# Optimization experiments

Hardware: AMD Instinct MI355X
Metric: run time of the kernel (lower is better)

The kernel has to match this reference:

```python
import jax, jax.numpy as jnp
import numpy as np

N_INST = 524288   # total instances across all bags
NF = 256          # feature dim
L = 128           # gated-attention hidden dim
C = 1             # num_classes
B = 4096          # num bags


def setup_inputs() -> dict:
    key = jax.random.key(0)
    k = jax.random.split(key, 6)
    # ragged bag sizes averaging ~128, deterministically summing to N_INST
    rng = np.random.RandomState(0)
    raw = rng.randint(64, 193, size=B).astype(np.int64)
    sizes = (raw * N_INST // raw.sum()).astype(np.int64)
    sizes[: int(N_INST - sizes.sum())] += 1  # distribute remainder (< B)
    assert sizes.sum() == N_INST
    s = 1.0 / np.sqrt(NF)
    return {
        "feats": jax.random.normal(k[0], (N_INST, NF), jnp.float32),
        "split_sizes": jnp.asarray(sizes, jnp.int64),
        "W_ins": jax.random.normal(k[1], (NF, C), jnp.float32) * s,
        "b_ins": jnp.zeros((C,), jnp.float32),
        "W_V": jax.random.normal(k[2], (NF, L), jnp.float32) * s,
        "b_V": jnp.zeros((L,), jnp.float32),
        "W_U": jax.random.normal(k[3], (NF, L), jnp.float32) * s,
        "b_U": jnp.zeros((L,), jnp.float32),
        "w_att": jax.random.normal(k[4], (L, 1), jnp.float32) * (1.0 / np.sqrt(L)),
        "b_att": jnp.zeros((1,), jnp.float32),
    }


def reference(feats, split_sizes, W_ins, b_ins, W_V, b_V, W_U, b_U, w_att, b_att):
    n = feats.shape[0]
    num_bags = split_sizes.shape[0]
    # segment id per instance (fused replacement of torch.split + Python loop)
    seg = jnp.repeat(jnp.arange(num_bags), split_sizes, total_repeat_length=n)

    # instance classifier (applied once to the whole ragged batch)
    inst_pred = feats @ W_ins + b_ins                      # [N, C]

    # gated attention scores
    gate = jnp.tanh(feats @ W_V + b_V) * jax.nn.sigmoid(feats @ W_U + b_U)
    scores = (gate @ w_att + b_att)[:, 0]                  # [N]

    # segmented softmax over each bag
    m = jax.ops.segment_max(scores, seg, num_segments=num_bags)  # [B]
    e = jnp.exp(scores - m[seg])
    denom = jax.ops.segment_sum(e, seg, num_segments=num_bags)   # [B]
    attn = e / denom[seg]                                        # [N]

    # bag prediction = attention-weighted sum of instance predictions
    bag_pred = jax.ops.segment_sum(attn[:, None] * inst_pred, seg,
                                   num_segments=num_bags)        # [B, C]
    return bag_pred, inst_pred
```

## Files before the change

### kernel.cpp

```cpp
#include <hip/hip_runtime.h>
#include <hip/hip_bf16.h>

#define N_INST 524288
#define NF     256
#define LDIM   128
#define NBAGS  4096
#define BM     128

typedef __attribute__((ext_vector_type(8)))  short          short8;
typedef __attribute__((ext_vector_type(16))) float          f32x16;
typedef __attribute__((ext_vector_type(4)))  unsigned short ushort4v;
typedef __attribute__((ext_vector_type(4)))  int            int4v;

__device__ __forceinline__ unsigned short f2bf(float f) {
    unsigned u = __float_as_uint(f);
    unsigned r = u + 0x7FFFu + ((u >> 16) & 1u);
    return (unsigned short)(r >> 16);
}

__global__ __launch_bounds__(256) void k_build(const float* __restrict__ W_V,
                                               const float* __restrict__ W_U,
                                               unsigned short* __restrict__ Bws) {
    int idx  = blockIdx.x * 256 + threadIdx.x;
    int j    = idx & 7;
    int lane = (idx >> 3) & 63;
    int ct   = (idx >> 9) & 7;
    int ks   = idx >> 12;
    int k    = ks * 16 + ((lane >> 5) << 3) + j;
    int n    = ((ct >> 1) << 5) + (lane & 31);
    const float* src = (ct & 1) ? W_U : W_V;
    Bws[idx] = f2bf(src[k * LDIM + n]);
}

__global__ __launch_bounds__(256) void k_scan(const int* __restrict__ sraw,
                                              int* __restrict__ offs) {
    __shared__ int csum[256];
    __shared__ int cpref[256];
    const int t = threadIdx.x;
    const bool is64 = (sraw[1] == 0);
    int local[16];
    int ssum = 0;
    for (int j = 0; j < 16; ++j) {
        int i = t * 16 + j;
        int v = is64 ? sraw[2 * i] : sraw[i];
        local[j] = v;
        ssum += v;
    }
    csum[t] = ssum;
    __syncthreads();
    if (t == 0) {
        int run = 0;
        for (int i = 0; i < 256; ++i) { cpref[i] = run; run += csum[i]; }
    }
    __syncthreads();
    int run = cpref[t];
    for (int j = 0; j < 16; ++j) { offs[t * 16 + j] = run; run += local[j]; }
    if (t == 255) offs[NBAGS] = run;
}

__global__ __launch_bounds__(256, 2) void k_gemm(
    const float* __restrict__ feats, const unsigned short* __restrict__ Bws,
    const float* __restrict__ W_ins, const float* __restrict__ b_ins,
    const float* __restrict__ b_V,   const float* __restrict__ b_U,
    const float* __restrict__ w_att, const float* __restrict__ b_att,
    float* __restrict__ scores, float* __restrict__ inst_out) {

    __shared__ unsigned short Al[2][2048];
    __shared__ unsigned short Bl[2][4096];
    __shared__ float winsl[NF];
    __shared__ float bVl[LDIM], bUl[LDIM], wal[LDIM];
    __shared__ float Sp[BM][4];

    const int t    = threadIdx.x;
    const int lane = t & 63;
    const int cg   = t >> 6;
    const long r0  = (long)blockIdx.x * BM;

    const int row0 = t >> 2;
    const int q    = t & 3;
    const int row1 = row0 + 64;

    winsl[t] = W_ins[t];
    if (t < LDIM) { bVl[t] = b_V[t]; bUl[t] = b_U[t]; wal[t] = w_att[t]; }

    const float* arow0 = feats + (r0 + row0) * NF + q * 4;
    const float* arow1 = feats + (r0 + row1) * NF + q * 4;
    const int4v* bsrc  = (const int4v*)Bws;

    const int aoff0 = ((row0 >> 5) * 64 + (q >> 1) * 32 + (row0 & 31)) * 8 + (q & 1) * 4;
    const int aoff1 = ((row1 >> 5) * 64 + (q >> 1) * 32 + (row1 & 31)) * 8 + (q & 1) * 4;

    float4 pa0_0 = *(const float4*)(arow0);
    float4 pa1_0 = *(const float4*)(arow1);
    int4v  pb0_0 = bsrc[t];
    int4v  pb1_0 = bsrc[t + 256];
    float4 pa0_1 = *(const float4*)(arow0 + 16);
    float4 pa1_1 = *(const float4*)(arow1 + 16);
    int4v  pb0_1 = bsrc[512 + t];
    int4v  pb1_1 = bsrc[512 + t + 256];

    f32x16 accV0 = {}, accV1 = {}, accV2 = {}, accV3 = {};
    f32x16 accU0 = {}, accU1 = {}, accU2 = {}, accU3 = {};
    float pacc0 = 0.f, pacc1 = 0.f;

    __syncthreads();

    #pragma unroll
    for (int ks = 0; ks < 16; ++ks) {
        float4 av0 = (ks & 1) ? pa0_1 : pa0_0;
        float4 av1 = (ks & 1) ? pa1_1 : pa1_0;
        int4v  bv0 = (ks & 1) ? pb0_1 : pb0_0;
        int4v  bv1 = (ks & 1) ? pb1_1 : pb1_0;
        const int X = ks & 1;

        float4 wv = *(const float4*)&winsl[ks * 16 + q * 4];
        pacc0 += av0.x * wv.x + av0.y * wv.y + av0.z * wv.z + av0.w * wv.w;
        pacc1 += av1.x * wv.x + av1.y * wv.y + av1.z * wv.z + av1.w * wv.w;

        ushort4v c0, c1;
        c0.x = f2bf(av0.x); c0.y = f2bf(av0.y); c0.z = f2bf(av0.z); c0.w = f2bf(av0.w);
        c1.x = f2bf(av1.x); c1.y = f2bf(av1.y); c1.z = f2bf(av1.z); c1.w = f2bf(av1.w);
        *(ushort4v*)&Al[X][aoff0] = c0;
        *(ushort4v*)&Al[X][aoff1] = c1;
        ((int4v*)Bl[X])[t]       = bv0;
        ((int4v*)Bl[X])[t + 256] = bv1;

        if (ks < 14) {
            if (X == 0) {
                pa0_0 = *(const float4*)(arow0 + (ks + 2) * 16);
                pa1_0 = *(const float4*)(arow1 + (ks + 2) * 16);
                pb0_0 = bsrc[(ks + 2) * 512 + t];
                pb1_0 = bsrc[(ks + 2) * 512 + t + 256];
            } else {
                pa0_1 = *(const float4*)(arow0 + (ks + 2) * 16);
                pa1_1 = *(const float4*)(arow1 + (ks + 2) * 16);
                pb0_1 = bsrc[(ks + 2) * 512 + t];
                pb1_1 = bsrc[(ks + 2) * 512 + t + 256];
            }
        }

        __syncthreads();

        short8 fa0 = *(const short8*)&Al[X][(0 * 64 + lane) * 8];
        short8 fa1 = *(const short8*)&Al[X][(1 * 64 + lane) * 8];
        short8 fa2 = *(const short8*)&Al[X][(2 * 64 + lane) * 8];
        short8 fa3 = *(const short8*)&Al[X][(3 * 64 + lane) * 8];
        short8 fbv = *(const short8*)&Bl[X][((cg * 2 + 0) * 64 + lane) * 8];
        short8 fbu = *(const short8*)&Bl[X][((cg * 2 + 1) * 64 + lane) * 8];
        accV0 = __builtin_amdgcn_mfma_f32_32x32x16_bf16(fa0, fbv, accV0, 0, 0, 0);
        accU0 = __builtin_amdgcn_mfma_f32_32x32x16_bf16(fa0, fbu, accU0, 0, 0, 0);
        accV1 = __builtin_amdgcn_mfma_f32_32x32x16_bf16(fa1, fbv, accV1, 0, 0, 0);
        accU1 = __builtin_amdgcn_mfma_f32_32x32x16_bf16(fa1, fbu, accU1, 0, 0, 0);
        accV2 = __builtin_amdgcn_mfma_f32_32x32x16_bf16(fa2, fbv, accV2, 0, 0, 0);
        accU2 = __builtin_amdgcn_mfma_f32_32x32x16_bf16(fa2, fbu, accU2, 0, 0, 0);
        accV3 = __builtin_amdgcn_mfma_f32_32x32x16_bf16(fa3, fbv, accV3, 0, 0, 0);
        accU3 = __builtin_amdgcn_mfma_f32_32x32x16_bf16(fa3, fbu, accU3, 0, 0, 0);
    }

    const int   c32 = lane & 31;
    const int   nn  = cg * 32 + c32;
    const float bv0s = bVl[nn], bu0s = bUl[nn], wn = wal[nn];
    const int   rh  = lane >> 5;

#define EPILOG(RT, AV, AU)                                                    \
    {                                                                         \
        _Pragma("unroll")                                                     \
        for (int r = 0; r < 16; ++r) {                                        \
            float v  = AV[r] + bv0s;                                          \
            float u  = AU[r] + bu0s;                                          \
            float ev = __expf(2.f * v);                                       \
            float th = 1.f - 2.f * __builtin_amdgcn_rcpf(ev + 1.f);           \
            float sg = __builtin_amdgcn_rcpf(1.f + __expf(-u));               \
            float x  = th * sg * wn;                                          \
            x += __shfl_xor(x, 1);                                            \
            x += __shfl_xor(x, 2);                                            \
            x += __shfl_xor(x, 4);                                            \
            x += __shfl_xor(x, 8);                                            \
            x += __shfl_xor(x, 16);                                           \
            if (c32 == 0)                                                     \
                Sp[RT * 32 + (r & 3) + 8 * (r >> 2) + 4 * rh][cg] = x;        \
        }                                                                     \
    }
    EPILOG(0, accV0, accU0)
    EPILOG(1, accV1, accU1)
    EPILOG(2, accV2, accU2)
    EPILOG(3, accV3, accU3)
#undef EPILOG

    float pt0 = pacc0;
    pt0 += __shfl_xor(pt0, 1);
    pt0 += __shfl_xor(pt0, 2);
    float pt1 = pacc1;
    pt1 += __shfl_xor(pt1, 1);
    pt1 += __shfl_xor(pt1, 2);
    if (q == 0) {
        float bi = b_ins[0];
        inst_out[r0 + row0] = pt0 + bi;
        inst_out[r0 + row1] = pt1 + bi;
    }

    __syncthreads();
    if (t < BM)
        scores[r0 + t] = Sp[t][0] + Sp[t][1] + Sp[t][2] + Sp[t][3] + b_att[0];
}

__global__ __launch_bounds__(64) void k_bags(const int* __restrict__ offs,
                                             const float* __restrict__ scores,
                                             const float* __restrict__ inst,
                                             float* __restrict__ bag_out) {
    const int b    = blockIdx.x;
    const int lane = threadIdx.x;
    const int s0 = offs[b], s1 = offs[b + 1];
    float m = -1e30f;
    for (int i = s0 + lane; i < s1; i += 64) m = fmaxf(m, scores[i]);
    #pragma unroll
    for (int d = 32; d; d >>= 1) m = fmaxf(m, __shfl_xor(m, d));
    float se = 0.f, sp = 0.f;
    for (int i = s0 + lane; i < s1; i += 64) {
        float e = __expf(scores[i] - m);
        se += e;
        sp += e * inst[i];
    }
    #pragma unroll
    for (int d = 32; d; d >>= 1) { se += __shfl_xor(se, d); sp += __shfl_xor(sp, d); }
    if (lane == 0) bag_out[b] = sp / se;
}

extern "C" void kernel_launch(void* const* d_in, const int* in_sizes, int n_in,
                              void* d_out, int out_size, void* d_ws, size_t ws_size,
                              hipStream_t stream) {
    const float* feats  = (const float*)d_in[0];
    const int*   sizesr = (const int*)d_in[1];
    const float* W_ins  = (const float*)d_in[2];
    const float* b_ins  = (const float*)d_in[3];
    const float* W_V    = (const float*)d_in[4];
    const float* b_V    = (const float*)d_in[5];
    const float* W_U    = (const float*)d_in[6];
    const float* b_U    = (const float*)d_in[7];
    const float* w_att  = (const float*)d_in[8];
    const float* b_att  = (const float*)d_in[9];

    unsigned short* Bws    = (unsigned short*)d_ws;
    int*            offs   = (int*)((char*)d_ws + (128 << 10));
    float*          scores = (float*)((char*)d_ws + (160 << 10));

    float* bag_out  = (float*)d_out;
    float* inst_out = (float*)d_out + NBAGS;

    hipLaunchKernelGGL(k_build, dim3(256), dim3(256), 0, stream, W_V, W_U, Bws);
    hipLaunchKernelGGL(k_scan,  dim3(1),   dim3(256), 0, stream, sizesr, offs);
    hipLaunchKernelGGL(k_gemm,  dim3(N_INST / BM), dim3(256), 0, stream,
                       feats, Bws, W_ins, b_ins, b_V, b_U, w_att, b_att,
                       scores, inst_out);
    hipLaunchKernelGGL(k_bags,  dim3(NBAGS), dim3(64), 0, stream,
                       offs, scores, inst_out, bag_out);
}
```

Before: 886.1 us.

## Halve GEMM row tile and load B fragments directly from global into registers

The row tile of the fused gated-attention GEMM drops from 128 to 64 instances per block. Each wave now loads its bf16 weight fragments straight from global memory into registers, with no shared-memory B staging, and occupancy is raised to 3 blocks per SIMD. This removes the LDS traffic and stores for B, lowers accumulator register pressure, and doubles the grid to improve latency hiding. In exchange, weight reuse per block is halved, so more global/L2 reads of B are needed per instance.

```diff
diff --git a/kernel.cpp b/kernel.cpp
--- a/kernel.cpp
+++ b/kernel.cpp
@@ -5,7 +5,7 @@
 #define NF     256
 #define LDIM   128
 #define NBAGS  4096
-#define BM     128
+#define BM     64
 
 typedef __attribute__((ext_vector_type(8)))  short          short8;
 typedef __attribute__((ext_vector_type(16))) float          f32x16;
@@ -58,15 +58,14 @@
     if (t == 255) offs[NBAGS] = run;
 }
 
-__global__ __launch_bounds__(256, 2) void k_gemm(
+__global__ __launch_bounds__(256, 3) void k_gemm(
     const float* __restrict__ feats, const unsigned short* __restrict__ Bws,
     const float* __restrict__ W_ins, const float* __restrict__ b_ins,
     const float* __restrict__ b_V,   const float* __restrict__ b_U,
     const float* __restrict__ w_att, const float* __restrict__ b_att,
     float* __restrict__ scores, float* __restrict__ inst_out) {
 
-    __shared__ unsigned short Al[2][2048];
-    __shared__ unsigned short Bl[2][4096];
+    __shared__ unsigned short Al[2][1024];
     __shared__ float winsl[NF];
     __shared__ float bVl[LDIM], bUl[LDIM], wal[LDIM];
     __shared__ float Sp[BM][4];
@@ -76,66 +75,55 @@
     const int cg   = t >> 6;
     const long r0  = (long)blockIdx.x * BM;
 
-    const int row0 = t >> 2;
-    const int q    = t & 3;
-    const int row1 = row0 + 64;
+    const int row = t >> 2;
+    const int q   = t & 3;
 
     winsl[t] = W_ins[t];
     if (t < LDIM) { bVl[t] = b_V[t]; bUl[t] = b_U[t]; wal[t] = w_att[t]; }
 
-    const float* arow0 = feats + (r0 + row0) * NF + q * 4;
-    const float* arow1 = feats + (r0 + row1) * NF + q * 4;
-    const int4v* bsrc  = (const int4v*)Bws;
-
-    const int aoff0 = ((row0 >> 5) * 64 + (q >> 1) * 32 + (row0 & 31)) * 8 + (q & 1) * 4;
-    const int aoff1 = ((row1 >> 5) * 64 + (q >> 1) * 32 + (row1 & 31)) * 8 + (q & 1) * 4;
-
-    float4 pa0_0 = *(const float4*)(arow0);
-    float4 pa1_0 = *(const float4*)(arow1);
-    int4v  pb0_0 = bsrc[t];
-    int4v  pb1_0 = bsrc[t + 256];
-    float4 pa0_1 = *(const float4*)(arow0 + 16);
-    float4 pa1_1 = *(const float4*)(arow1 + 16);
-    int4v  pb0_1 = bsrc[512 + t];
-    int4v  pb1_1 = bsrc[512 + t + 256];
-
-    f32x16 accV0 = {}, accV1 = {}, accV2 = {}, accV3 = {};
-    f32x16 accU0 = {}, accU1 = {}, accU2 = {}, accU3 = {};
-    float pacc0 = 0.f, pacc1 = 0.f;
+    const float*  arow = feats + (r0 + row) * NF + q * 4;
+    const short8* bw   = (const short8*)Bws;
+
+    const int aoff = ((row >> 5) * 64 + (q >> 1) * 32 + (row & 31)) * 8 + (q & 1) * 4;
+    const int ctv  = cg * 2;
+    const int ctu  = ctv + 1;
+
+    float4 pa_0  = *(const float4*)(arow);
+    short8 fbv_0 = bw[(0 * 8 + ctv) * 64 + lane];
+    short8 fbu_0 = bw[(0 * 8 + ctu) * 64 + lane];
+    float4 pa_1  = *(const float4*)(arow + 16);
+    short8 fbv_1 = bw[(1 * 8 + ctv) * 64 + lane];
+    short8 fbu_1 = bw[(1 * 8 + ctu) * 64 + lane];
+
+    f32x16 accV0 = {}, accV1 = {};
+    f32x16 accU0 = {}, accU1 = {};
+    float pacc = 0.f;
 
     __syncthreads();
 
     #pragma unroll
     for (int ks = 0; ks < 16; ++ks) {
-        float4 av0 = (ks & 1) ? pa0_1 : pa0_0;
-        float4 av1 = (ks & 1) ? pa1_1 : pa1_0;
-        int4v  bv0 = (ks & 1) ? pb0_1 : pb0_0;
-        int4v  bv1 = (ks & 1) ? pb1_1 : pb1_0;
         const int X = ks & 1;
+        float4 av  = X ? pa_1  : pa_0;
+        short8 fbv = X ? fbv_1 : fbv_0;
+        short8 fbu = X ? fbu_1 : fbu_0;
 
         float4 wv = *(const float4*)&winsl[ks * 16 + q * 4];
-        pacc0 += av0.x * wv.x + av0.y * wv.y + av0.z * wv.z + av0.w * wv.w;
-        pacc1 += av1.x * wv.x + av1.y * wv.y + av1.z * wv.z + av1.w * wv.w;
-
-        ushort4v c0, c1;
-        c0.x = f2bf(av0.x); c0.y = f2bf(av0.y); c0.z = f2bf(av0.z); c0.w = f2bf(av0.w);
-        c1.x = f2bf(av1.x); c1.y = f2bf(av1.y); c1.z = f2bf(av1.z); c1.w = f2bf(av1.w);
-        *(ushort4v*)&Al[X][aoff0] = c0;
-        *(ushort4v*)&Al[X][aoff1] = c1;
-        ((int4v*)Bl[X])[t]       = bv0;
-        ((int4v*)Bl[X])[t + 256] = bv1;
+        pacc += av.x * wv.x + av.y * wv.y + av.z * wv.z + av.w * wv.w;
+
+        ushort4v c;
+        c.x = f2bf(av.x); c.y = f2bf(av.y); c.z = f2bf(av.z); c.w = f2bf(av.w);
+        *(ushort4v*)&Al[X][aoff] = c;
 
         if (ks < 14) {
             if (X == 0) {
-                pa0_0 = *(const float4*)(arow0 + (ks + 2) * 16);
-                pa1_0 = *(const float4*)(arow1 + (ks + 2) * 16);
-                pb0_0 = bsrc[(ks + 2) * 512 + t];
-                pb1_0 = bsrc[(ks + 2) * 512 + t + 256];
+                pa_0  = *(const float4*)(arow + (ks + 2) * 16);
+                fbv_0 = bw[((ks + 2) * 8 + ctv) * 64 + lane];
+                fbu_0 = bw[((ks + 2) * 8 + ctu) * 64 + lane];
             } else {
-                pa0_1 = *(const float4*)(arow0 + (ks + 2) * 16);
-                pa1_1 = *(const float4*)(arow1 + (ks + 2) * 16);
-                pb0_1 = bsrc[(ks + 2) * 512 + t];
-                pb1_1 = bsrc[(ks + 2) * 512 + t + 256];
+                pa_1  = *(const float4*)(arow + (ks + 2) * 16);
+                fbv_1 = bw[((ks + 2) * 8 + ctv) * 64 + lane];
+                fbu_1 = bw[((ks + 2) * 8 + ctu) * 64 + lane];
             }
         }
 
@@ -143,18 +131,10 @@
 
         short8 fa0 = *(const short8*)&Al[X][(0 * 64 + lane) * 8];
         short8 fa1 = *(const short8*)&Al[X][(1 * 64 + lane) * 8];
-        short8 fa2 = *(const short8*)&Al[X][(2 * 64 + lane) * 8];
-        short8 fa3 = *(const short8*)&Al[X][(3 * 64 + lane) * 8];
-        short8 fbv = *(const short8*)&Bl[X][((cg * 2 + 0) * 64 + lane) * 8];
-        short8 fbu = *(const short8*)&Bl[X][((cg * 2 + 1) * 64 + lane) * 8];
         accV0 = __builtin_amdgcn_mfma_f32_32x32x16_bf16(fa0, fbv, accV0, 0, 0, 0);
         accU0 = __builtin_amdgcn_mfma_f32_32x32x16_bf16(fa0, fbu, accU0, 0, 0, 0);
         accV1 = __builtin_amdgcn_mfma_f32_32x32x16_bf16(fa1, fbv, accV1, 0, 0, 0);
         accU1 = __builtin_amdgcn_mfma_f32_32x32x16_bf16(fa1, fbu, accU1, 0, 0, 0);
-        accV2 = __builtin_amdgcn_mfma_f32_32x32x16_bf16(fa2, fbv, accV2, 0, 0, 0);
-        accU2 = __builtin_amdgcn_mfma_f32_32x32x16_bf16(fa2, fbu, accU2, 0, 0, 0);
-        accV3 = __builtin_amdgcn_mfma_f32_32x32x16_bf16(fa3, fbv, accV3, 0, 0, 0);
-        accU3 = __builtin_amdgcn_mfma_f32_32x32x16_bf16(fa3, fbu, accU3, 0, 0, 0);
     }
 
     const int   c32 = lane & 31;
@@ -183,21 +163,12 @@
     }
     EPILOG(0, accV0, accU0)
     EPILOG(1, accV1, accU1)
-    EPILOG(2, accV2, accU2)
-    EPILOG(3, accV3, accU3)
 #undef EPILOG
 
-    float pt0 = pacc0;
-    pt0 += __shfl_xor(pt0, 1);
-    pt0 += __shfl_xor(pt0, 2);
-    float pt1 = pacc1;
-    pt1 += __shfl_xor(pt1, 1);
-    pt1 += __shfl_xor(pt1, 2);
-    if (q == 0) {
-        float bi = b_ins[0];
-        inst_out[r0 + row0] = pt0 + bi;
-        inst_out[r0 + row1] = pt1 + bi;
-    }
+    float pt = pacc;
+    pt += __shfl_xor(pt, 1);
+    pt += __shfl_xor(pt, 2);
+    if (q == 0) inst_out[r0 + row] = pt + b_ins[0];
 
     __syncthreads();
     if (t < BM)
```

Result: no change. 898.1 us (+1.4%).
